# Performance work log

Hardware: AMD Instinct MI355X
Metric: run time of the kernel (lower is better)

The kernel has to match this reference:

```python
import jax, jax.numpy as jnp
import numpy as np

MARGIN = 1.0
EPS = 1e-08


def setup_inputs() -> dict:
    key = jax.random.key(0)
    k0, k1 = jax.random.split(key)
    kernels0 = jax.random.normal(k0, (2048, 3, 3), dtype=jnp.float32)
    kernels1 = jax.random.normal(k1, (1024, 5, 5), dtype=jnp.float32)
    return {"kernels0": kernels0, "kernels1": kernels1}


def _layer_loss(kernels):
    n, d, _ = kernels.shape
    # Frobenius-normalize each kernel
    norms = jnp.sqrt(jnp.sum(kernels * kernels, axis=(1, 2), keepdims=True)) + EPS
    kn = kernels / norms                      # (n, d, d)
    inv = jnp.linalg.inv(kn)                  # (n, d, d)
    # AB[i, j] = inv[i] @ kn[j]; BA[i, j] = inv[j] @ kn[i]
    ab = jnp.einsum('iab,jbc->ijac', inv, kn)  # (n, n, d, d)
    ba = jnp.einsum('jab,ibc->ijac', inv, kn)  # (n, n, d, d)
    eye = jnp.eye(d, dtype=kernels.dtype)
    diff_ab = jnp.sqrt(jnp.sum((eye - ab) ** 2, axis=(2, 3)))  # (n, n)
    diff_ba = jnp.sqrt(jnp.sum((eye - ba) ** 2, axis=(2, 3)))  # (n, n)
    combined = jnp.tril(diff_ab) + jnp.triu(diff_ba)
    loss_mat = jax.nn.relu(MARGIN - combined)
    mask = ~jnp.eye(n, dtype=bool)
    loss_mat = jnp.where(mask, loss_mat, 0.0)
    return jnp.sum(loss_mat) / (n * (n - 1))


def reference(kernels0, kernels1):
    losses = [_layer_loss(kernels0), _layer_loss(kernels1)]
    return sum(losses) / len(losses)
```

## Files before the change

kernel.cpp:

```cpp
#include <hip/hip_runtime.h>
#include <math.h>

#define N0 2048
#define N1 1024
#define M0T 32
#define M1T 32
#define NB0 (M0T * (M0T + 1) / 2)
#define NB1 (M1T * (M1T + 1) / 2)
#define NBTOT (NB0 + NB1)


__global__ __launch_bounds__(64) void prep_kernel(const float* __restrict__ k0,
                                                  const float* __restrict__ k1,
                                                  float* __restrict__ kn0,
                                                  float* __restrict__ inv0,
                                                  float* __restrict__ kn1,
                                                  float* __restrict__ inv1) {
    int t = blockIdx.x * blockDim.x + threadIdx.x;
    if (t < N0) {
        float a[9];
        float ss = 0.0f;
#pragma unroll
        for (int e = 0; e < 9; ++e) { a[e] = k0[t * 9 + e]; ss = fmaf(a[e], a[e], ss); }
        float rn = 1.0f / (sqrtf(ss) + 1e-8f);
#pragma unroll
        for (int e = 0; e < 9; ++e) a[e] *= rn;
        float c00 = a[4] * a[8] - a[5] * a[7];
        float c01 = -(a[3] * a[8] - a[5] * a[6]);
        float c02 = a[3] * a[7] - a[4] * a[6];
        float det = a[0] * c00 + a[1] * c01 + a[2] * c02;
        float id = 1.0f / det;
        float x[9];
        x[0] = c00 * id;
        x[1] = (a[2] * a[7] - a[1] * a[8]) * id;
        x[2] = (a[1] * a[5] - a[2] * a[4]) * id;
        x[3] = c01 * id;
        x[4] = (a[0] * a[8] - a[2] * a[6]) * id;
        x[5] = (a[2] * a[3] - a[0] * a[5]) * id;
        x[6] = c02 * id;
        x[7] = (a[1] * a[6] - a[0] * a[7]) * id;
        x[8] = (a[0] * a[4] - a[1] * a[3]) * id;
        float r[9];
#pragma unroll
        for (int i = 0; i < 3; ++i)
#pragma unroll
            for (int j = 0; j < 3; ++j) {
                float m = a[i * 3 + 0] * x[0 * 3 + j];
                m = fmaf(a[i * 3 + 1], x[1 * 3 + j], m);
                m = fmaf(a[i * 3 + 2], x[2 * 3 + j], m);
                r[i * 3 + j] = ((i == j) ? 2.0f : 0.0f) - m;
            }
        float xn[9];
#pragma unroll
        for (int i = 0; i < 3; ++i)
#pragma unroll
            for (int j = 0; j < 3; ++j) {
                float m = x[i * 3 + 0] * r[0 * 3 + j];
                m = fmaf(x[i * 3 + 1], r[1 * 3 + j], m);
                m = fmaf(x[i * 3 + 2], r[2 * 3 + j], m);
                xn[i * 3 + j] = m;
            }
#pragma unroll
        for (int e = 0; e < 9; ++e) {
            kn0[t * 9 + e] = a[e];
            inv0[t * 9 + e] = xn[e];
        }
    } else {
        int u = t - N0;
        if (u < N1) {
            float A[5][5], B[5][5], K[5][5];
            float ss = 0.0f;
#pragma unroll
            for (int r = 0; r < 5; ++r)
#pragma unroll
                for (int c = 0; c < 5; ++c) {
                    float v = k1[u * 25 + r * 5 + c];
                    A[r][c] = v;
                    ss = fmaf(v, v, ss);
                }
            float rn = 1.0f / (sqrtf(ss) + 1e-8f);
#pragma unroll
            for (int r = 0; r < 5; ++r)
#pragma unroll
                for (int c = 0; c < 5; ++c) {
                    A[r][c] *= rn;
                    K[r][c] = A[r][c];
                    kn1[u * 25 + r * 5 + c] = A[r][c];
                    B[r][c] = (r == c) ? 1.0f : 0.0f;
                }
#pragma unroll
            for (int k = 0; k < 5; ++k) {
#pragma unroll
                for (int r = k + 1; r < 5; ++r) {
                    bool sw = fabsf(A[r][k]) > fabsf(A[k][k]);
#pragma unroll
                    for (int c = k; c < 5; ++c) {
                        float Ar = A[r][c], Ak = A[k][c];
                        A[r][c] = sw ? Ak : Ar;
                        A[k][c] = sw ? Ar : Ak;
                    }
#pragma unroll
                    for (int c = 0; c < 5; ++c) {
                        float Br = B[r][c], Bk = B[k][c];
                        B[r][c] = sw ? Bk : Br;
                        B[k][c] = sw ? Br : Bk;
                    }
                }
                float piv = 1.0f / A[k][k];
#pragma unroll
                for (int c = k; c < 5; ++c) A[k][c] *= piv;
#pragma unroll
                for (int c = 0; c < 5; ++c) B[k][c] *= piv;
#pragma unroll
                for (int r = 0; r < 5; ++r) {
                    if (r == k) continue;
                    float f = A[r][k];
#pragma unroll
                    for (int c = k; c < 5; ++c) A[r][c] = fmaf(-f, A[k][c], A[r][c]);
#pragma unroll
                    for (int c = 0; c < 5; ++c) B[r][c] = fmaf(-f, B[k][c], B[r][c]);
                }
            }
            float R[5][5];
#pragma unroll
            for (int i = 0; i < 5; ++i)
#pragma unroll
                for (int j = 0; j < 5; ++j) {
                    float m = K[i][0] * B[0][j];
#pragma unroll
                    for (int k = 1; k < 5; ++k) m = fmaf(K[i][k], B[k][j], m);
                    R[i][j] = ((i == j) ? 2.0f : 0.0f) - m;
                }
#pragma unroll
            for (int i = 0; i < 5; ++i)
#pragma unroll
                for (int j = 0; j < 5; ++j) {
                    float m = B[i][0] * R[0][j];
#pragma unroll
                    for (int k = 1; k < 5; ++k) m = fmaf(B[i][k], R[k][j], m);
                    inv1[u * 25 + i * 5 + j] = m;
                }
        }
    }
}

__global__ __launch_bounds__(256) void pairs_kernel(const float* __restrict__ inv0,
                                                    const float* __restrict__ kn0,
                                                    const float* __restrict__ inv1,
                                                    const float* __restrict__ kn1,
                                                    float* __restrict__ partial) {
    __shared__ float sA[800];
    __shared__ float sB[800];
    int tid = threadIdx.x;
    float contrib = 0.0f;

    if (blockIdx.x < NB0) {
        int t = blockIdx.x;
        int bi = (int)((sqrtf(8.0f * t + 1.0f) - 1.0f) * 0.5f);
        while ((bi + 1) * (bi + 2) / 2 <= t) ++bi;
        while (bi * (bi + 1) / 2 > t) --bi;
        int bj = t - bi * (bi + 1) / 2;

        for (int e = tid; e < 64 * 9; e += 256) {
            sA[e] = inv0[bi * 576 + e];
            sB[e] = kn0[bj * 576 + e];
        }
        __syncthreads();

        int ti = tid >> 4, tj = tid & 15;
        int ibase = bi * 64 + ti * 4, jbase = bj * 64 + tj * 4;
        float a[4][9];
#pragma unroll
        for (int u = 0; u < 4; ++u)
#pragma unroll
            for (int e = 0; e < 9; ++e) a[u][e] = sA[(ti * 4 + u) * 9 + e];
#pragma unroll
        for (int v = 0; v < 4; ++v) {
            float b[9];
#pragma unroll
            for (int e = 0; e < 9; ++e) b[e] = sB[(tj * 4 + v) * 9 + e];
#pragma unroll
            for (int u = 0; u < 4; ++u) {
                float s = 0.0f;
#pragma unroll
                for (int r = 0; r < 3; ++r)
#pragma unroll
                    for (int c = 0; c < 3; ++c) {
                        float m = a[u][r * 3 + 0] * b[c];
                        m = fmaf(a[u][r * 3 + 1], b[3 + c], m);
                        m = fmaf(a[u][r * 3 + 2], b[6 + c], m);
                        float d = ((r == c) ? 1.0f : 0.0f) - m;
                        s = fmaf(d, d, s);
                    }
                bool take = ((ibase + u) > (jbase + v)) && (s < 1.0f);
                contrib += take ? (1.0f - sqrtf(s)) : 0.0f;
            }
        }
    } else {
        int t = blockIdx.x - NB0;
        int bi = (int)((sqrtf(8.0f * t + 1.0f) - 1.0f) * 0.5f);
        while ((bi + 1) * (bi + 2) / 2 <= t) ++bi;
        while (bi * (bi + 1) / 2 > t) --bi;
        int bj = t - bi * (bi + 1) / 2;

        for (int e = tid; e < 32 * 25; e += 256) {
            sA[e] = inv1[bi * 800 + e];
            sB[e] = kn1[bj * 800 + e];
        }
        __syncthreads();

        int ti = tid >> 4, tj = tid & 15;
        int ibase = bi * 32 + ti * 2, jbase = bj * 32 + tj * 2;
        float a[2][25];
#pragma unroll
        for (int u = 0; u < 2; ++u)
#pragma unroll
            for (int e = 0; e < 25; ++e) a[u][e] = sA[(ti * 2 + u) * 25 + e];
#pragma unroll
        for (int v = 0; v < 2; ++v) {
            float b[25];
#pragma unroll
            for (int e = 0; e < 25; ++e) b[e] = sB[(tj * 2 + v) * 25 + e];
#pragma unroll
            for (int u = 0; u < 2; ++u) {
                float s = 0.0f;
#pragma unroll
                for (int r = 0; r < 5; ++r)
#pragma unroll
                    for (int c = 0; c < 5; ++c) {
                        float m = a[u][r * 5 + 0] * b[c];
#pragma unroll
                        for (int k = 1; k < 5; ++k) m = fmaf(a[u][r * 5 + k], b[k * 5 + c], m);
                        float d = ((r == c) ? 1.0f : 0.0f) - m;
                        s = fmaf(d, d, s);
                    }
                bool take = ((ibase + u) > (jbase + v)) && (s < 1.0f);
                contrib += take ? (1.0f - sqrtf(s)) : 0.0f;
            }
        }
    }

#pragma unroll
    for (int off = 32; off; off >>= 1) contrib += __shfl_down(contrib, off);
    __shared__ float wsum[4];
    if ((tid & 63) == 0) wsum[tid >> 6] = contrib;
    __syncthreads();
    if (tid == 0) partial[blockIdx.x] = wsum[0] + wsum[1] + wsum[2] + wsum[3];
}

__global__ void finalize_kernel(const float* __restrict__ partial, float* __restrict__ out) {
    int tid = threadIdx.x;
    double s0 = 0.0, s1 = 0.0;
    for (int x = tid; x < NB0; x += 256) s0 += (double)partial[x];
    for (int x = NB0 + tid; x < NBTOT; x += 256) s1 += (double)partial[x];
#pragma unroll
    for (int off = 32; off; off >>= 1) {
        s0 += __shfl_down(s0, off);
        s1 += __shfl_down(s1, off);
    }
    __shared__ double w0[4], w1[4];
    if ((tid & 63) == 0) { w0[tid >> 6] = s0; w1[tid >> 6] = s1; }
    __syncthreads();
    if (tid == 0) {
        double S0 = w0[0] + w0[1] + w0[2] + w0[3];
        double S1 = w1[0] + w1[1] + w1[2] + w1[3];
        double res = S0 / ((double)N0 * (double)(N0 - 1)) +
                     S1 / ((double)N1 * (double)(N1 - 1));
        out[0] = (float)res;
    }
}

extern "C" void kernel_launch(void* const* d_in, const int* in_sizes, int n_in,
                              void* d_out, int out_size, void* d_ws, size_t ws_size,
                              hipStream_t stream) {
    const float* k0 = (const float*)d_in[0];
    const float* k1 = (const float*)d_in[1];
    float* out = (float*)d_out;

    float* ws = (float*)d_ws;
    float* kn0 = ws;
    float* inv0 = kn0 + N0 * 9;
    float* kn1 = inv0 + N0 * 9;
    float* inv1 = kn1 + N1 * 25;
    float* partial = inv1 + N1 * 25;

    int totalPrep = N0 + N1;
    prep_kernel<<<(totalPrep + 63) / 64, 64, 0, stream>>>(k0, k1, kn0, inv0, kn1, inv1);

    pairs_kernel<<<NBTOT, 256, 0, stream>>>(inv0, kn0, inv1, kn1, partial);

    finalize_kernel<<<1, 256, 0, stream>>>(partial, out);
}
```

Baseline: 69.75 us.

## Fuse prep, pair and finalize kernels into one with atomic last-block reduction

Drops the separate prep kernel. Each pair block now normalizes its own kernels and computes their inverses straight into shared memory. The finalize kernel is replaced by per-block double atomic adds and a counter, so the last block writes the result; a memset clears the accumulators first. This removes two kernel launches and the workspace round trip, at the cost of redundant inversion work (each tile is recomputed by about 32 blocks) and serial per-thread inversion before the block barrier.

New measurement: 87.24 us. +25.1%, slower.

```diff
diff --git a/kernel.cpp b/kernel.cpp
--- a/kernel.cpp
+++ b/kernel.cpp
@@ -10,160 +10,167 @@
 #define NBTOT (NB0 + NB1)
 
 
-__global__ __launch_bounds__(64) void prep_kernel(const float* __restrict__ k0,
-                                                  const float* __restrict__ k1,
-                                                  float* __restrict__ kn0,
-                                                  float* __restrict__ inv0,
-                                                  float* __restrict__ kn1,
-                                                  float* __restrict__ inv1) {
-    int t = blockIdx.x * blockDim.x + threadIdx.x;
-    if (t < N0) {
-        float a[9];
-        float ss = 0.0f;
-#pragma unroll
-        for (int e = 0; e < 9; ++e) { a[e] = k0[t * 9 + e]; ss = fmaf(a[e], a[e], ss); }
-        float rn = 1.0f / (sqrtf(ss) + 1e-8f);
-#pragma unroll
-        for (int e = 0; e < 9; ++e) a[e] *= rn;
-        float c00 = a[4] * a[8] - a[5] * a[7];
-        float c01 = -(a[3] * a[8] - a[5] * a[6]);
-        float c02 = a[3] * a[7] - a[4] * a[6];
-        float det = a[0] * c00 + a[1] * c01 + a[2] * c02;
-        float id = 1.0f / det;
-        float x[9];
-        x[0] = c00 * id;
-        x[1] = (a[2] * a[7] - a[1] * a[8]) * id;
-        x[2] = (a[1] * a[5] - a[2] * a[4]) * id;
-        x[3] = c01 * id;
-        x[4] = (a[0] * a[8] - a[2] * a[6]) * id;
-        x[5] = (a[2] * a[3] - a[0] * a[5]) * id;
-        x[6] = c02 * id;
-        x[7] = (a[1] * a[6] - a[0] * a[7]) * id;
-        x[8] = (a[0] * a[4] - a[1] * a[3]) * id;
-        float r[9];
-#pragma unroll
-        for (int i = 0; i < 3; ++i)
-#pragma unroll
-            for (int j = 0; j < 3; ++j) {
-                float m = a[i * 3 + 0] * x[0 * 3 + j];
-                m = fmaf(a[i * 3 + 1], x[1 * 3 + j], m);
-                m = fmaf(a[i * 3 + 2], x[2 * 3 + j], m);
-                r[i * 3 + j] = ((i == j) ? 2.0f : 0.0f) - m;
-            }
-        float xn[9];
-#pragma unroll
-        for (int i = 0; i < 3; ++i)
-#pragma unroll
-            for (int j = 0; j < 3; ++j) {
-                float m = x[i * 3 + 0] * r[0 * 3 + j];
-                m = fmaf(x[i * 3 + 1], r[1 * 3 + j], m);
-                m = fmaf(x[i * 3 + 2], r[2 * 3 + j], m);
-                xn[i * 3 + j] = m;
-            }
-#pragma unroll
-        for (int e = 0; e < 9; ++e) {
-            kn0[t * 9 + e] = a[e];
-            inv0[t * 9 + e] = xn[e];
-        }
-    } else {
-        int u = t - N0;
-        if (u < N1) {
-            float A[5][5], B[5][5], K[5][5];
-            float ss = 0.0f;
-#pragma unroll
-            for (int r = 0; r < 5; ++r)
-#pragma unroll
-                for (int c = 0; c < 5; ++c) {
-                    float v = k1[u * 25 + r * 5 + c];
-                    A[r][c] = v;
-                    ss = fmaf(v, v, ss);
-                }
-            float rn = 1.0f / (sqrtf(ss) + 1e-8f);
-#pragma unroll
-            for (int r = 0; r < 5; ++r)
-#pragma unroll
-                for (int c = 0; c < 5; ++c) {
-                    A[r][c] *= rn;
-                    K[r][c] = A[r][c];
-                    kn1[u * 25 + r * 5 + c] = A[r][c];
-                    B[r][c] = (r == c) ? 1.0f : 0.0f;
-                }
-#pragma unroll
-            for (int k = 0; k < 5; ++k) {
-#pragma unroll
-                for (int r = k + 1; r < 5; ++r) {
-                    bool sw = fabsf(A[r][k]) > fabsf(A[k][k]);
-#pragma unroll
-                    for (int c = k; c < 5; ++c) {
-                        float Ar = A[r][c], Ak = A[k][c];
-                        A[r][c] = sw ? Ak : Ar;
-                        A[k][c] = sw ? Ar : Ak;
-                    }
-#pragma unroll
-                    for (int c = 0; c < 5; ++c) {
-                        float Br = B[r][c], Bk = B[k][c];
-                        B[r][c] = sw ? Bk : Br;
-                        B[k][c] = sw ? Br : Bk;
-                    }
-                }
-                float piv = 1.0f / A[k][k];
-#pragma unroll
-                for (int c = k; c < 5; ++c) A[k][c] *= piv;
-#pragma unroll
-                for (int c = 0; c < 5; ++c) B[k][c] *= piv;
-#pragma unroll
-                for (int r = 0; r < 5; ++r) {
-                    if (r == k) continue;
-                    float f = A[r][k];
-#pragma unroll
-                    for (int c = k; c < 5; ++c) A[r][c] = fmaf(-f, A[k][c], A[r][c]);
-#pragma unroll
-                    for (int c = 0; c < 5; ++c) B[r][c] = fmaf(-f, B[k][c], B[r][c]);
-                }
-            }
-            float R[5][5];
-#pragma unroll
-            for (int i = 0; i < 5; ++i)
-#pragma unroll
-                for (int j = 0; j < 5; ++j) {
-                    float m = K[i][0] * B[0][j];
-#pragma unroll
-                    for (int k = 1; k < 5; ++k) m = fmaf(K[i][k], B[k][j], m);
-                    R[i][j] = ((i == j) ? 2.0f : 0.0f) - m;
-                }
-#pragma unroll
-            for (int i = 0; i < 5; ++i)
-#pragma unroll
-                for (int j = 0; j < 5; ++j) {
-                    float m = B[i][0] * R[0][j];
-#pragma unroll
-                    for (int k = 1; k < 5; ++k) m = fmaf(B[i][k], R[k][j], m);
-                    inv1[u * 25 + i * 5 + j] = m;
-                }
+
+__device__ __forceinline__ void inv3_newton(const float* __restrict__ src, float* __restrict__ out) {
+    float a[9];
+    float ss = 0.0f;
+#pragma unroll
+    for (int e = 0; e < 9; ++e) { a[e] = src[e]; ss = fmaf(a[e], a[e], ss); }
+    float rn = 1.0f / (sqrtf(ss) + 1e-8f);
+#pragma unroll
+    for (int e = 0; e < 9; ++e) a[e] *= rn;
+    float c00 = a[4] * a[8] - a[5] * a[7];
+    float c01 = -(a[3] * a[8] - a[5] * a[6]);
+    float c02 = a[3] * a[7] - a[4] * a[6];
+    float det = a[0] * c00 + a[1] * c01 + a[2] * c02;
+    float id = 1.0f / det;
+    float x[9];
+    x[0] = c00 * id;
+    x[1] = (a[2] * a[7] - a[1] * a[8]) * id;
+    x[2] = (a[1] * a[5] - a[2] * a[4]) * id;
+    x[3] = c01 * id;
+    x[4] = (a[0] * a[8] - a[2] * a[6]) * id;
+    x[5] = (a[2] * a[3] - a[0] * a[5]) * id;
+    x[6] = c02 * id;
+    x[7] = (a[1] * a[6] - a[0] * a[7]) * id;
+    x[8] = (a[0] * a[4] - a[1] * a[3]) * id;
+    float r[9];
+#pragma unroll
+    for (int i = 0; i < 3; ++i)
+#pragma unroll
+        for (int j = 0; j < 3; ++j) {
+            float m = a[i * 3 + 0] * x[j];
+            m = fmaf(a[i * 3 + 1], x[3 + j], m);
+            m = fmaf(a[i * 3 + 2], x[6 + j], m);
+            r[i * 3 + j] = ((i == j) ? 2.0f : 0.0f) - m;
+        }
+#pragma unroll
+    for (int i = 0; i < 3; ++i)
+#pragma unroll
+        for (int j = 0; j < 3; ++j) {
+            float m = x[i * 3 + 0] * r[j];
+            m = fmaf(x[i * 3 + 1], r[3 + j], m);
+            m = fmaf(x[i * 3 + 2], r[6 + j], m);
+            out[i * 3 + j] = m;
+        }
+}
+
+__device__ __forceinline__ void norm3(const float* __restrict__ src, float* __restrict__ out) {
+    float a[9];
+    float ss = 0.0f;
+#pragma unroll
+    for (int e = 0; e < 9; ++e) { a[e] = src[e]; ss = fmaf(a[e], a[e], ss); }
+    float rn = 1.0f / (sqrtf(ss) + 1e-8f);
+#pragma unroll
+    for (int e = 0; e < 9; ++e) out[e] = a[e] * rn;
+}
+
+__device__ __forceinline__ void inv5_newton(const float* __restrict__ src, float* __restrict__ out) {
+    float A[5][5], B[5][5], K[5][5];
+    float ss = 0.0f;
+#pragma unroll
+    for (int r = 0; r < 5; ++r)
+#pragma unroll
+        for (int c = 0; c < 5; ++c) {
+            float v = src[r * 5 + c];
+            A[r][c] = v;
+            ss = fmaf(v, v, ss);
+        }
+    float rn = 1.0f / (sqrtf(ss) + 1e-8f);
+#pragma unroll
+    for (int r = 0; r < 5; ++r)
+#pragma unroll
+        for (int c = 0; c < 5; ++c) {
+            A[r][c] *= rn;
+            K[r][c] = A[r][c];
+            B[r][c] = (r == c) ? 1.0f : 0.0f;
+        }
+#pragma unroll
+    for (int k = 0; k < 5; ++k) {
+#pragma unroll
+        for (int r = k + 1; r < 5; ++r) {
+            bool sw = fabsf(A[r][k]) > fabsf(A[k][k]);
+#pragma unroll
+            for (int c = k; c < 5; ++c) {
+                float Ar = A[r][c], Ak = A[k][c];
+                A[r][c] = sw ? Ak : Ar;
+                A[k][c] = sw ? Ar : Ak;
+            }
+#pragma unroll
+            for (int c = 0; c < 5; ++c) {
+                float Br = B[r][c], Bk = B[k][c];
+                B[r][c] = sw ? Bk : Br;
+                B[k][c] = sw ? Br : Bk;
+            }
+        }
+        float piv = 1.0f / A[k][k];
+#pragma unroll
+        for (int c = k; c < 5; ++c) A[k][c] *= piv;
+#pragma unroll
+        for (int c = 0; c < 5; ++c) B[k][c] *= piv;
+#pragma unroll
+        for (int r = 0; r < 5; ++r) {
+            if (r == k) continue;
+            float f = A[r][k];
+#pragma unroll
+            for (int c = k; c < 5; ++c) A[r][c] = fmaf(-f, A[k][c], A[r][c]);
+#pragma unroll
+            for (int c = 0; c < 5; ++c) B[r][c] = fmaf(-f, B[k][c], B[r][c]);
         }
     }
-}
-
-__global__ __launch_bounds__(256) void pairs_kernel(const float* __restrict__ inv0,
-                                                    const float* __restrict__ kn0,
-                                                    const float* __restrict__ inv1,
-                                                    const float* __restrict__ kn1,
-                                                    float* __restrict__ partial) {
+    float R[5][5];
+#pragma unroll
+    for (int i = 0; i < 5; ++i)
+#pragma unroll
+        for (int j = 0; j < 5; ++j) {
+            float m = K[i][0] * B[0][j];
+#pragma unroll
+            for (int k = 1; k < 5; ++k) m = fmaf(K[i][k], B[k][j], m);
+            R[i][j] = ((i == j) ? 2.0f : 0.0f) - m;
+        }
+#pragma unroll
+    for (int i = 0; i < 5; ++i)
+#pragma unroll
+        for (int j = 0; j < 5; ++j) {
+            float m = B[i][0] * R[0][j];
+#pragma unroll
+            for (int k = 1; k < 5; ++k) m = fmaf(B[i][k], R[k][j], m);
+            out[i * 5 + j] = m;
+        }
+}
+
+__device__ __forceinline__ void norm5(const float* __restrict__ src, float* __restrict__ out) {
+    float a[25];
+    float ss = 0.0f;
+#pragma unroll
+    for (int e = 0; e < 25; ++e) { a[e] = src[e]; ss = fmaf(a[e], a[e], ss); }
+    float rn = 1.0f / (sqrtf(ss) + 1e-8f);
+#pragma unroll
+    for (int e = 0; e < 25; ++e) out[e] = a[e] * rn;
+}
+
+__global__ __launch_bounds__(256) void fused_kernel(const float* __restrict__ k0,
+                                                    const float* __restrict__ k1,
+                                                    double* __restrict__ acc,
+                                                    float* __restrict__ out) {
     __shared__ float sA[800];
     __shared__ float sB[800];
     int tid = threadIdx.x;
     float contrib = 0.0f;
-
-    if (blockIdx.x < NB0) {
+    bool isL0 = blockIdx.x < NB0;
+
+    if (isL0) {
         int t = blockIdx.x;
         int bi = (int)((sqrtf(8.0f * t + 1.0f) - 1.0f) * 0.5f);
         while ((bi + 1) * (bi + 2) / 2 <= t) ++bi;
         while (bi * (bi + 1) / 2 > t) --bi;
         int bj = t - bi * (bi + 1) / 2;
 
-        for (int e = tid; e < 64 * 9; e += 256) {
-            sA[e] = inv0[bi * 576 + e];
-            sB[e] = kn0[bj * 576 + e];
+        if (tid < 64) {
+            inv3_newton(&k0[(bi * 64 + tid) * 9], &sA[tid * 9]);
+        } else if (tid < 128) {
+            int m = tid - 64;
+            norm3(&k0[(bj * 64 + m) * 9], &sB[m * 9]);
         }
         __syncthreads();
 
@@ -203,9 +210,11 @@
         while (bi * (bi + 1) / 2 > t) --bi;
         int bj = t - bi * (bi + 1) / 2;
 
-        for (int e = tid; e < 32 * 25; e += 256) {
-            sA[e] = inv1[bi * 800 + e];
-            sB[e] = kn1[bj * 800 + e];
+        if (tid < 32) {
+            inv5_newton(&k1[(bi * 32 + tid) * 25], &sA[tid * 25]);
+        } else if (tid >= 64 && tid < 96) {
+            int m = tid - 64;
+            norm5(&k1[(bj * 32 + m) * 25], &sB[m * 25]);
         }
         __syncthreads();
 
@@ -245,28 +254,21 @@
     __shared__ float wsum[4];
     if ((tid & 63) == 0) wsum[tid >> 6] = contrib;
     __syncthreads();
-    if (tid == 0) partial[blockIdx.x] = wsum[0] + wsum[1] + wsum[2] + wsum[3];
-}
-
-__global__ void finalize_kernel(const float* __restrict__ partial, float* __restrict__ out) {
-    int tid = threadIdx.x;
-    double s0 = 0.0, s1 = 0.0;
-    for (int x = tid; x < NB0; x += 256) s0 += (double)partial[x];
-    for (int x = NB0 + tid; x < NBTOT; x += 256) s1 += (double)partial[x];
-#pragma unroll
-    for (int off = 32; off; off >>= 1) {
-        s0 += __shfl_down(s0, off);
-        s1 += __shfl_down(s1, off);
-    }
-    __shared__ double w0[4], w1[4];
-    if ((tid & 63) == 0) { w0[tid >> 6] = s0; w1[tid >> 6] = s1; }
-    __syncthreads();
+
     if (tid == 0) {
-        double S0 = w0[0] + w0[1] + w0[2] + w0[3];
-        double S1 = w1[0] + w1[1] + w1[2] + w1[3];
-        double res = S0 / ((double)N0 * (double)(N0 - 1)) +
-                     S1 / ((double)N1 * (double)(N1 - 1));
-        out[0] = (float)res;
+        double bs = (double)(wsum[0] + wsum[1] + wsum[2] + wsum[3]);
+        atomicAdd(&acc[isL0 ? 0 : 1], bs);
+        __threadfence();
+        unsigned int* cnt = (unsigned int*)(acc + 2);
+        unsigned int old = atomicAdd(cnt, 1u);
+        if (old == NBTOT - 1) {
+            __threadfence();
+            double S0 = atomicAdd(&acc[0], 0.0);
+            double S1 = atomicAdd(&acc[1], 0.0);
+            double res = S0 / ((double)N0 * (double)(N0 - 1)) +
+                         S1 / ((double)N1 * (double)(N1 - 1));
+            out[0] = (float)res;
+        }
     }
 }
 
@@ -276,18 +278,8 @@
     const float* k0 = (const float*)d_in[0];
     const float* k1 = (const float*)d_in[1];
     float* out = (float*)d_out;
-
-    float* ws = (float*)d_ws;
-    float* kn0 = ws;
-    float* inv0 = kn0 + N0 * 9;
-    float* kn1 = inv0 + N0 * 9;
-    float* inv1 = kn1 + N1 * 25;
-    float* partial = inv1 + N1 * 25;
-
-    int totalPrep = N0 + N1;
-    prep_kernel<<<(totalPrep + 63) / 64, 64, 0, stream>>>(k0, k1, kn0, inv0, kn1, inv1);
-
-    pairs_kernel<<<NBTOT, 256, 0, stream>>>(inv0, kn0, inv1, kn1, partial);
-
-    finalize_kernel<<<1, 256, 0, stream>>>(partial, out);
-}
+    double* acc = (double*)d_ws;
+
+    hipMemsetAsync(acc, 0, 24, stream);
+    fused_kernel<<<NBTOT, 256, 0, stream>>>(k0, k1, acc, out);
+}
```
